# Optimization experiments

Hardware: AMD Instinct MI355X
Metric: run time of the kernel (lower is better)

## Reference

```python
import jax, jax.numpy as jnp
import numpy as np
from jax import lax

_DN = ('NCHW', 'OIHW', 'NCHW')


def _box1(s, k):
    # Separable box sum (all-ones kxk kernel) on a single-channel map (B,1,H,W).
    pad = (k - 1) // 2
    kh = jnp.ones((1, 1, k, 1), s.dtype)
    kw = jnp.ones((1, 1, 1, k), s.dtype)
    y = lax.conv_general_dilated(s, kh, (1, 1), [(pad, pad), (0, 0)], dimension_numbers=_DN)
    return lax.conv_general_dilated(y, kw, (1, 1), [(0, 0), (pad, pad)], dimension_numbers=_DN)


def _cgf(x, y, k, eps):
    # ConvGuidedFilterDlicate with weight-1 Conv2d(C,C,k): every output channel of
    # box_filter(t) equals box_sum(t.sum(channels)), so we keep channel dim = 1 and broadcast.
    B, C, H, W = x.shape
    Nc = C * _box1(jnp.ones((1, 1, H, W), x.dtype), k)           # box_filter(ones(1,C,H,W))
    mean_x = _box1(x.sum(1, keepdims=True), k) / Nc              # (B,1,H,W)
    mean_y = _box1(y.sum(1, keepdims=True), k) / Nc
    cov_xy = _box1((x * y).sum(1, keepdims=True), k) / Nc - mean_x * mean_y
    var_x = _box1((x * x).sum(1, keepdims=True), k) / Nc - mean_x * mean_x
    A = cov_xy / (var_x + eps)
    b = mean_y - A * mean_x
    # torch's A/b have C identical channels; box_filter then sums them -> factor C.
    mean_A = C * _box1(A, k)
    mean_b = C * _box1(b, k)
    return mean_A * y + mean_b                                   # broadcasts to (B,C,H,W)


def setup_inputs() -> dict:
    key = jax.random.key(0)
    k1, k2 = jax.random.split(key)
    x_hr = jax.random.normal(k1, (16, 3, 512, 512), jnp.float32)
    w1 = jax.random.normal(k2, (3, 9), jnp.float32) * 0.1        # conv1 weight (O, 3*nin1)
    return {"x_hr": x_hr, "w1": w1}


def reference(x_hr, w1):
    F1 = _cgf(x_hr, x_hr, 3, 0.16)
    F2 = _cgf(F1, F1, 7, 0.04)
    F3 = _cgf(F2, F2, 15, 0.01)
    D = jnp.concatenate([x_hr - F1, F1 - F2, F2 - F3], axis=1)   # (B,9,H,W)
    return jnp.einsum('oi,bihw->bohw', w1, D)                    # 1x1 conv, no bias
```

## Files before the change

### kernel.cpp

```cpp
#include <hip/hip_runtime.h>

#define BB 16
#define CC 3
#define HH 512
#define WW 512
#define HWP (HH*WW)
#define NMAP ((size_t)BB*HWP)

template <int P, int CH, int MODE>
__global__ __launch_bounds__(512, (MODE == 3 ? 2 : 4))
void stage(const float* __restrict__ xin, const float2* __restrict__ sqin,
           float2* __restrict__ abo, float2* __restrict__ sqo,
           const float2* __restrict__ ab1, const float2* __restrict__ ab2,
           const float* __restrict__ w1, float* __restrict__ outp, float eps)
{
    constexpr int RD  = 2*P + 1;
    constexpr int LW  = 512 + 2*P;
    constexpr int NCH = HH / CH;
    __shared__ float2 eA[LW];
    __shared__ float2 eB[LW];

    const int t  = threadIdx.x;
    const int bx = blockIdx.x;
    const int b  = bx / NCH;
    const int h0 = (bx % NCH) * CH;
    const size_t mapbase = (size_t)b * HWP;
    const float*  xb  = (MODE != 2) ? (xin + (size_t)b * CC * HWP) : nullptr;
    const float2* sqb = (MODE != 1) ? (sqin + mapbase) : nullptr;

    if (t < 2*P) {
        int sl = (t < P) ? t : (512 + t);
        eA[sl] = make_float2(0.f, 0.f);
        eB[sl] = make_float2(0.f, 0.f);
    }

    const int w   = t;
    const int wlo = (w - P < 0) ? 0 : w - P;
    const int whi = (w + P > WW-1) ? WW-1 : w + P;
    const float rcw = 1.0f / (float)(whi - wlo + 1);

    float cs0 = 0.f, cs1 = 0.f;
    float ca  = 0.f, cb  = 0.f;
    float rA[RD], rB[RD];

    auto loadSQ = [&](int rr, float& sv, float& qv) {
        size_t o = (size_t)rr * WW + w;
        if constexpr (MODE == 1) {
            float x0 = xb[o], x1 = xb[o + HWP], x2 = xb[o + 2*HWP];
            sv = x0 + x1 + x2;
            qv = x0*x0 + x1*x1 + x2*x2;
        } else {
            float2 v = sqb[o];
            sv = v.x; qv = v.y;
        }
    };

    auto advance = [&](int r) {
        int rin = r + P, rout = r - P - 1;
        if (rin < HH)  { float sv, qv; loadSQ(rin,  sv, qv); cs0 += sv; cs1 += qv; }
        if (rout >= 0) { float sv, qv; loadSQ(rout, sv, qv); cs0 -= sv; cs1 -= qv; }
    };

    auto phase1 = [&](int r, float& Aout, float& Bout) {
        eA[t + P] = make_float2(cs0, cs1);
        __syncthreads();
        float hs0 = 0.f, hs1 = 0.f;
#pragma unroll
        for (int d = 0; d <= 2*P; ++d) { float2 v = eA[t + d]; hs0 += v.x; hs1 += v.y; }
        __syncthreads();
        int rlo = (r - P < 0) ? 0 : r - P;
        int rhi = (r + P > HH-1) ? HH-1 : r + P;
        float rNc  = (1.f/3.f) * rcw / (float)(rhi - rlo + 1);
        float mean = hs0 * rNc;
        float var  = hs1 * rNc - mean * mean;
        float A    = var / (var + eps);
        Aout = A;
        Bout = mean * (1.f - A);
    };

    float w1r[27];
    if constexpr (MODE == 3) {
#pragma unroll
        for (int k = 0; k < 27; ++k) w1r[k] = w1[k];
    }

#pragma unroll
    for (int d = 0; d <= 2*P; ++d) {
        int rr = h0 - 2*P + d;
        if (rr >= 0) { float sv, qv; loadSQ(rr, sv, qv); cs0 += sv; cs1 += qv; }
    }

#pragma unroll
    for (int j = 0; j < 2*P; ++j) {
        int r = h0 - P + j;
        if (j > 0) advance(r);
        float A = 0.f, Bv = 0.f;
        if (r >= 0) { phase1(r, A, Bv); ca += A; cb += Bv; }
        rA[j % RD] = A; rB[j % RD] = Bv;
    }

#pragma unroll
    for (int i = 0; i < CH; ++i) {
        int r = h0 + P + i;
        int h = h0 + i;
        advance(r);
        float A = 0.f, Bv = 0.f;
        if (r < HH) { phase1(r, A, Bv); ca += A; cb += Bv; }
        rA[(2*P + i) % RD] = A; rB[(2*P + i) % RD] = Bv;

        eB[t + P] = make_float2(ca, cb);
        __syncthreads();
        float sA = 0.f, sB = 0.f;
#pragma unroll
        for (int d = 0; d <= 2*P; ++d) { float2 v = eB[t + d]; sA += v.x; sB += v.y; }
        __syncthreads();

        size_t oi = mapbase + (size_t)h * WW + w;
        if constexpr (MODE != 3) {
            abo[oi] = make_float2(sA, sB);
            float sv, qv; loadSQ(h, sv, qv);
            float mA = 3.f * sA, mb = 3.f * sB;
            sqo[oi] = make_float2(mA*sv + 3.f*mb,
                                  mA*mA*qv + 2.f*mA*mb*sv + 3.f*mb*mb);
        } else {
            float a3 = 3.f*sA, b3 = 3.f*sB;
            float2 v1 = ab1[oi], v2 = ab2[oi];
            float a1 = 3.f*v1.x, b1 = 3.f*v1.y;
            float a2 = 3.f*v2.x, b2 = 3.f*v2.y;
            float P1 = a1,      Q1 = b1;
            float P2 = a2 * P1, Q2 = a2 * Q1 + b2;
            float P3 = a3 * P2, Q3 = a3 * Q2 + b3;
            float alpha[3] = {1.f - P1, P1 - P2, P2 - P3};
            float beta[3]  = {-Q1,      Q1 - Q2, Q2 - Q3};
            size_t xo = (size_t)h * WW + w;
            float xv0 = xb[xo], xv1 = xb[xo + HWP], xv2 = xb[xo + 2*HWP];
#pragma unroll
            for (int o = 0; o < 3; ++o) {
                float acc = 0.f;
#pragma unroll
                for (int g = 0; g < 3; ++g) {
                    float w0v = w1r[o*9 + g*3 + 0];
                    float wv1 = w1r[o*9 + g*3 + 1];
                    float w2v = w1r[o*9 + g*3 + 2];
                    acc += alpha[g] * (w0v*xv0 + wv1*xv1 + w2v*xv2)
                         + beta[g]  * (w0v + wv1 + w2v);
                }
                outp[(size_t)b * CC * HWP + (size_t)o * HWP + xo] = acc;
            }
        }
        ca -= rA[i % RD]; cb -= rB[i % RD];
    }
}

extern "C" void kernel_launch(void* const* d_in, const int* in_sizes, int n_in,
                              void* d_out, int out_size, void* d_ws, size_t ws_size,
                              hipStream_t stream) {
    (void)in_sizes; (void)n_in; (void)out_size; (void)ws_size;
    const float* x  = (const float*)d_in[0];
    const float* w1 = (const float*)d_in[1];
    float* out = (float*)d_out;

    float2* sq1 = (float2*)d_ws;
    float2* sq2 = sq1 + NMAP;
    float2* ab1 = sq2 + NMAP;
    float2* ab2 = ab1 + NMAP;

    dim3 bl(512);
    dim3 g(BB * (HH / 16));

    stage<1,16,1><<<g, bl, 0, stream>>>(x, nullptr, ab1, sq1,
                                        nullptr, nullptr, nullptr, nullptr, 0.16f);
    stage<3,16,2><<<g, bl, 0, stream>>>(nullptr, sq1, ab2, sq2,
                                        nullptr, nullptr, nullptr, nullptr, 0.04f);
    stage<7,16,3><<<g, bl, 0, stream>>>(x, sq2, nullptr, nullptr,
                                        ab1, ab2, w1, out, 0.01f);
}
```

Baseline: 220.7 us.

## Process two columns per thread and merge both box-filter passes into one sync round

Each thread now handles two adjacent columns with 256-thread blocks, using vectorised float2/float4 loads and stores. The horizontal box sums for the (sum, sq) statistics and for the (A, b) coefficients are computed from shared memory in a single sync pair per row instead of two. The loop is software-pipelined so the next row's global loads are issued before the shared-memory exchange. Stages 1 and 2 also move to 8-row chunks, which adds halo recomputation in exchange for more blocks.

```diff
diff --git a/kernel.cpp b/kernel.cpp
--- a/kernel.cpp
+++ b/kernel.cpp
@@ -8,17 +8,21 @@
 #define NMAP ((size_t)BB*HWP)
 
 template <int P, int CH, int MODE>
-__global__ __launch_bounds__(512, (MODE == 3 ? 2 : 4))
+__global__ __launch_bounds__(256, MODE == 3 ? 2 : 4)
 void stage(const float* __restrict__ xin, const float2* __restrict__ sqin,
            float2* __restrict__ abo, float2* __restrict__ sqo,
-           const float2* __restrict__ ab1, const float2* __restrict__ ab2,
-           const float* __restrict__ w1, float* __restrict__ outp, float eps)
+           const float2* __restrict__ abp1, const float2* __restrict__ abp2,
+           const float* __restrict__ wt, float* __restrict__ outp, float eps)
 {
     constexpr int RD  = 2*P + 1;
-    constexpr int LW  = 512 + 2*P;
+    constexpr int HE  = (P+1)/2;
+    constexpr int NIT = CH + 2*P + 1;
     constexpr int NCH = HH / CH;
-    __shared__ float2 eA[LW];
-    __shared__ float2 eB[LW];
+    constexpr int mm  = (P-1)/2;
+    constexpr int MM  = (P+1)/2;
+
+    __shared__ float4 ev[256 + 2*HE];
+    __shared__ float4 od[256 + 2*HE];
 
     const int t  = threadIdx.x;
     const int bx = blockIdx.x;
@@ -28,127 +32,163 @@
     const float*  xb  = (MODE != 2) ? (xin + (size_t)b * CC * HWP) : nullptr;
     const float2* sqb = (MODE != 1) ? (sqin + mapbase) : nullptr;
 
-    if (t < 2*P) {
-        int sl = (t < P) ? t : (512 + t);
-        eA[sl] = make_float2(0.f, 0.f);
-        eB[sl] = make_float2(0.f, 0.f);
-    }
-
-    const int w   = t;
-    const int wlo = (w - P < 0) ? 0 : w - P;
-    const int whi = (w + P > WW-1) ? WW-1 : w + P;
-    const float rcw = 1.0f / (float)(whi - wlo + 1);
-
-    float cs0 = 0.f, cs1 = 0.f;
-    float ca  = 0.f, cb  = 0.f;
-    float rA[RD], rB[RD];
-
-    auto loadSQ = [&](int rr, float& sv, float& qv) {
-        size_t o = (size_t)rr * WW + w;
+    if (t < 2*HE) {
+        int sl = (t < HE) ? t : 256 + t;
+        ev[sl] = make_float4(0.f, 0.f, 0.f, 0.f);
+        od[sl] = make_float4(0.f, 0.f, 0.f, 0.f);
+    }
+
+    const int wc0 = 2*t;
+    const int wc1 = wc0 + 1;
+    const int wlo0 = (wc0-P < 0) ? 0 : wc0-P, whi0 = (wc0+P > WW-1) ? WW-1 : wc0+P;
+    const int wlo1 = (wc1-P < 0) ? 0 : wc1-P, whi1 = (wc1+P > WW-1) ? WW-1 : wc1+P;
+    const float rcw0 = 1.0f / (float)(whi0 - wlo0 + 1);
+    const float rcw1 = 1.0f / (float)(whi1 - wlo1 + 1);
+
+    float2 cs0 = make_float2(0.f,0.f), cs1 = make_float2(0.f,0.f);
+    float2 ca0 = make_float2(0.f,0.f), ca1 = make_float2(0.f,0.f);
+    float2 rg0[RD], rg1[RD];
+#pragma unroll
+    for (int k = 0; k < RD; ++k) { rg0[k] = make_float2(0.f,0.f); rg1[k] = make_float2(0.f,0.f); }
+
+    auto loadrow = [&](int rr, float2& d0, float2& d1) {
         if constexpr (MODE == 1) {
-            float x0 = xb[o], x1 = xb[o + HWP], x2 = xb[o + 2*HWP];
-            sv = x0 + x1 + x2;
-            qv = x0*x0 + x1*x1 + x2*x2;
+            size_t o = (size_t)rr * WW + wc0;
+            float2 x0 = *(const float2*)(xb + o);
+            float2 x1 = *(const float2*)(xb + o + HWP);
+            float2 x2 = *(const float2*)(xb + o + 2*HWP);
+            d0 = make_float2(x0.x+x1.x+x2.x, x0.x*x0.x + x1.x*x1.x + x2.x*x2.x);
+            d1 = make_float2(x0.y+x1.y+x2.y, x0.y*x0.y + x1.y*x1.y + x2.y*x2.y);
         } else {
-            float2 v = sqb[o];
-            sv = v.x; qv = v.y;
+            float4 v = ((const float4*)(sqb + (size_t)rr * WW))[t];
+            d0 = make_float2(v.x, v.y);
+            d1 = make_float2(v.z, v.w);
         }
     };
 
-    auto advance = [&](int r) {
-        int rin = r + P, rout = r - P - 1;
-        if (rin < HH)  { float sv, qv; loadSQ(rin,  sv, qv); cs0 += sv; cs1 += qv; }
-        if (rout >= 0) { float sv, qv; loadSQ(rout, sv, qv); cs0 -= sv; cs1 -= qv; }
-    };
-
-    auto phase1 = [&](int r, float& Aout, float& Bout) {
-        eA[t + P] = make_float2(cs0, cs1);
-        __syncthreads();
-        float hs0 = 0.f, hs1 = 0.f;
-#pragma unroll
-        for (int d = 0; d <= 2*P; ++d) { float2 v = eA[t + d]; hs0 += v.x; hs1 += v.y; }
-        __syncthreads();
-        int rlo = (r - P < 0) ? 0 : r - P;
-        int rhi = (r + P > HH-1) ? HH-1 : r + P;
-        float rNc  = (1.f/3.f) * rcw / (float)(rhi - rlo + 1);
-        float mean = hs0 * rNc;
-        float var  = hs1 * rNc - mean * mean;
-        float A    = var / (var + eps);
-        Aout = A;
-        Bout = mean * (1.f - A);
-    };
+#pragma unroll
+    for (int d = 0; d <= 2*P; ++d) {
+        int rr = h0 - 2*P + d;
+        if (rr >= 0) {
+            float2 d0, d1; loadrow(rr, d0, d1);
+            cs0.x += d0.x; cs0.y += d0.y; cs1.x += d1.x; cs1.y += d1.y;
+        }
+    }
 
     float w1r[27];
     if constexpr (MODE == 3) {
 #pragma unroll
-        for (int k = 0; k < 27; ++k) w1r[k] = w1[k];
-    }
-
-#pragma unroll
-    for (int d = 0; d <= 2*P; ++d) {
-        int rr = h0 - 2*P + d;
-        if (rr >= 0) { float sv, qv; loadSQ(rr, sv, qv); cs0 += sv; cs1 += qv; }
-    }
-
-#pragma unroll
-    for (int j = 0; j < 2*P; ++j) {
-        int r = h0 - P + j;
-        if (j > 0) advance(r);
-        float A = 0.f, Bv = 0.f;
-        if (r >= 0) { phase1(r, A, Bv); ca += A; cb += Bv; }
-        rA[j % RD] = A; rB[j % RD] = Bv;
-    }
-
-#pragma unroll
-    for (int i = 0; i < CH; ++i) {
-        int r = h0 + P + i;
-        int h = h0 + i;
-        advance(r);
-        float A = 0.f, Bv = 0.f;
-        if (r < HH) { phase1(r, A, Bv); ca += A; cb += Bv; }
-        rA[(2*P + i) % RD] = A; rB[(2*P + i) % RD] = Bv;
-
-        eB[t + P] = make_float2(ca, cb);
+        for (int k = 0; k < 27; ++k) w1r[k] = wt[k];
+    }
+
+#pragma unroll
+    for (int j = 0; j < NIT; ++j) {
+        const int r = h0 - P + j;
+
+        float2 gi0 = make_float2(0.f,0.f), gi1 = make_float2(0.f,0.f);
+        float2 go0 = make_float2(0.f,0.f), go1 = make_float2(0.f,0.f);
+        if (j < NIT-1) {
+            int rin = r + 1 + P, rout = r - P;
+            if (rin < HH)  loadrow(rin, gi0, gi1);
+            if (rout >= 0) loadrow(rout, go0, go1);
+        }
+
+        ev[HE+t] = make_float4(cs0.x, cs0.y, ca0.x, ca0.y);
+        od[HE+t] = make_float4(cs1.x, cs1.y, ca1.x, ca1.y);
         __syncthreads();
-        float sA = 0.f, sB = 0.f;
-#pragma unroll
-        for (int d = 0; d <= 2*P; ++d) { float2 v = eB[t + d]; sA += v.x; sB += v.y; }
+
+        float4 CE = make_float4(0.f,0.f,0.f,0.f), CO = make_float4(0.f,0.f,0.f,0.f);
+#pragma unroll
+        for (int i = -mm; i <= mm; ++i) {
+            float4 e = ev[HE+t+i], o = od[HE+t+i];
+            CE.x += e.x; CE.y += e.y; CE.z += e.z; CE.w += e.w;
+            CO.x += o.x; CO.y += o.y; CO.z += o.z; CO.w += o.w;
+        }
+        float4 eM = ev[HE+t+MM], oM = od[HE+t-MM];
         __syncthreads();
 
-        size_t oi = mapbase + (size_t)h * WW + w;
-        if constexpr (MODE != 3) {
-            abo[oi] = make_float2(sA, sB);
-            float sv, qv; loadSQ(h, sv, qv);
-            float mA = 3.f * sA, mb = 3.f * sB;
-            sqo[oi] = make_float2(mA*sv + 3.f*mb,
-                                  mA*mA*qv + 2.f*mA*mb*sv + 3.f*mb*mb);
-        } else {
-            float a3 = 3.f*sA, b3 = 3.f*sB;
-            float2 v1 = ab1[oi], v2 = ab2[oi];
-            float a1 = 3.f*v1.x, b1 = 3.f*v1.y;
-            float a2 = 3.f*v2.x, b2 = 3.f*v2.y;
-            float P1 = a1,      Q1 = b1;
-            float P2 = a2 * P1, Q2 = a2 * Q1 + b2;
-            float P3 = a3 * P2, Q3 = a3 * Q2 + b3;
-            float alpha[3] = {1.f - P1, P1 - P2, P2 - P3};
-            float beta[3]  = {-Q1,      Q1 - Q2, Q2 - Q3};
-            size_t xo = (size_t)h * WW + w;
-            float xv0 = xb[xo], xv1 = xb[xo + HWP], xv2 = xb[xo + 2*HWP];
-#pragma unroll
-            for (int o = 0; o < 3; ++o) {
-                float acc = 0.f;
-#pragma unroll
-                for (int g = 0; g < 3; ++g) {
-                    float w0v = w1r[o*9 + g*3 + 0];
-                    float wv1 = w1r[o*9 + g*3 + 1];
-                    float w2v = w1r[o*9 + g*3 + 2];
-                    acc += alpha[g] * (w0v*xv0 + wv1*xv1 + w2v*xv2)
-                         + beta[g]  * (w0v + wv1 + w2v);
+        float4 S0 = make_float4(CE.x+CO.x+oM.x, CE.y+CO.y+oM.y, CE.z+CO.z+oM.z, CE.w+CO.w+oM.w);
+        float4 S1 = make_float4(CE.x+CO.x+eM.x, CE.y+CO.y+eM.y, CE.z+CO.z+eM.z, CE.w+CO.w+eM.w);
+
+        if (j >= 2*P+1) {
+            const int h = r - P - 1;
+            const size_t oi = (size_t)h * WW + wc0;
+            if constexpr (MODE != 3) {
+                *((float4*)(abo + mapbase + oi)) = make_float4(S0.z, S0.w, S1.z, S1.w);
+                float2 d0, d1; loadrow(h, d0, d1);
+                float mA0 = 3.f*S0.z, mb0 = 3.f*S0.w;
+                float mA1 = 3.f*S1.z, mb1 = 3.f*S1.w;
+                *((float4*)(sqo + mapbase + oi)) = make_float4(
+                    mA0*d0.x + 3.f*mb0,
+                    mA0*mA0*d0.y + 2.f*mA0*mb0*d0.x + 3.f*mb0*mb0,
+                    mA1*d1.x + 3.f*mb1,
+                    mA1*mA1*d1.y + 2.f*mA1*mb1*d1.x + 3.f*mb1*mb1);
+            } else {
+                float4 v1 = *((const float4*)(abp1 + mapbase + oi));
+                float4 v2 = *((const float4*)(abp2 + mapbase + oi));
+                float2 xc0 = *(const float2*)(xb + oi);
+                float2 xc1 = *(const float2*)(xb + oi + HWP);
+                float2 xc2 = *(const float2*)(xb + oi + 2*HWP);
+                float res0[3], res1[3];
+#pragma unroll
+                for (int c = 0; c < 2; ++c) {
+                    float a1 = 3.f * (c ? v1.z : v1.x), b1 = 3.f * (c ? v1.w : v1.y);
+                    float a2 = 3.f * (c ? v2.z : v2.x), b2 = 3.f * (c ? v2.w : v2.y);
+                    float a3 = 3.f * (c ? S1.z : S0.z), b3 = 3.f * (c ? S1.w : S0.w);
+                    float x0 = c ? xc0.y : xc0.x;
+                    float x1 = c ? xc1.y : xc1.x;
+                    float x2 = c ? xc2.y : xc2.x;
+                    float Pp1 = a1,       Q1 = b1;
+                    float Pp2 = a2 * Pp1, Q2 = a2 * Q1 + b2;
+                    float Pp3 = a3 * Pp2, Q3 = a3 * Q2 + b3;
+                    float al[3] = {1.f - Pp1, Pp1 - Pp2, Pp2 - Pp3};
+                    float be[3] = {-Q1,       Q1 - Q2,   Q2 - Q3};
+                    float* rr_ = c ? res1 : res0;
+#pragma unroll
+                    for (int o = 0; o < 3; ++o) {
+                        float acc = 0.f;
+#pragma unroll
+                        for (int g = 0; g < 3; ++g) {
+                            float wa = w1r[o*9 + g*3 + 0];
+                            float wb = w1r[o*9 + g*3 + 1];
+                            float wc = w1r[o*9 + g*3 + 2];
+                            acc += al[g] * (wa*x0 + wb*x1 + wc*x2)
+                                 + be[g] * (wa + wb + wc);
+                        }
+                        rr_[o] = acc;
+                    }
                 }
-                outp[(size_t)b * CC * HWP + (size_t)o * HWP + xo] = acc;
+                float* ob = outp + (size_t)b * CC * HWP + oi;
+#pragma unroll
+                for (int o = 0; o < 3; ++o)
+                    *((float2*)(ob + (size_t)o * HWP)) = make_float2(res0[o], res1[o]);
             }
         }
-        ca -= rA[i % RD]; cb -= rB[i % RD];
+
+        if (j < NIT-1) {
+            float2 A0 = make_float2(0.f,0.f), A1 = make_float2(0.f,0.f);
+            if ((unsigned)r < (unsigned)HH) {
+                const int rlo = (r-P < 0) ? 0 : r-P;
+                const int rhi = (r+P > HH-1) ? HH-1 : r+P;
+                const float rch = 1.0f / (float)(rhi - rlo + 1);
+                const float rN0 = (1.f/3.f) * rcw0 * rch;
+                const float rN1 = (1.f/3.f) * rcw1 * rch;
+                float mean0 = S0.x * rN0;
+                float var0  = S0.y * rN0 - mean0*mean0;
+                float a0    = var0 / (var0 + eps);
+                A0 = make_float2(a0, mean0 * (1.f - a0));
+                float mean1 = S1.x * rN1;
+                float var1  = S1.y * rN1 - mean1*mean1;
+                float a1v   = var1 / (var1 + eps);
+                A1 = make_float2(a1v, mean1 * (1.f - a1v));
+            }
+            const int ri = j % RD;
+            ca0.x += A0.x - rg0[ri].x; ca0.y += A0.y - rg0[ri].y;
+            ca1.x += A1.x - rg1[ri].x; ca1.y += A1.y - rg1[ri].y;
+            rg0[ri] = A0; rg1[ri] = A1;
+            cs0.x += gi0.x - go0.x; cs0.y += gi0.y - go0.y;
+            cs1.x += gi1.x - go1.x; cs1.y += gi1.y - go1.y;
+        }
     }
 }
 
@@ -165,13 +205,12 @@
     float2* ab1 = sq2 + NMAP;
     float2* ab2 = ab1 + NMAP;
 
-    dim3 bl(512);
-    dim3 g(BB * (HH / 16));
-
-    stage<1,16,1><<<g, bl, 0, stream>>>(x, nullptr, ab1, sq1,
+    dim3 bl(256);
+
+    stage<1,8,1><<<dim3(BB*(HH/8)), bl, 0, stream>>>(x, nullptr, ab1, sq1,
                                         nullptr, nullptr, nullptr, nullptr, 0.16f);
-    stage<3,16,2><<<g, bl, 0, stream>>>(nullptr, sq1, ab2, sq2,
+    stage<3,8,2><<<dim3(BB*(HH/8)), bl, 0, stream>>>(nullptr, sq1, ab2, sq2,
                                         nullptr, nullptr, nullptr, nullptr, 0.04f);
-    stage<7,16,3><<<g, bl, 0, stream>>>(x, sq2, nullptr, nullptr,
+    stage<7,16,3><<<dim3(BB*(HH/16)), bl, 0, stream>>>(x, sq2, nullptr, nullptr,
                                         ab1, ab2, w1, out, 0.01f);
 }
```

Measured after the change: 199.6 us. 9.6% less time.

## Fuse first two guided-filter stages into one pipelined kernel with 2 columns per thread

Applied to the files above, without the earlier changes.

Merges stages 1 and 2 into a single kernel that streams rows, computing stage-1 A/b and then feeding the stage-2 box sums in a row pipeline. This removes the intermediate sq1 map's global round trip and one launch. Each thread now handles two columns with vectorized float4 loads and stores, horizontal sums use double-buffered shared memory with one barrier per row, and block IDs are swizzled. The cost is higher register pressure, more halo recomputation across row chunks, and a more complex pipeline with more room for indexing errors.

```diff
diff --git a/kernel.cpp b/kernel.cpp
--- a/kernel.cpp
+++ b/kernel.cpp
@@ -1,154 +1,300 @@
 #include <hip/hip_runtime.h>
 
 #define BB 16
-#define CC 3
 #define HH 512
 #define WW 512
 #define HWP (HH*WW)
 #define NMAP ((size_t)BB*HWP)
 
-template <int P, int CH, int MODE>
-__global__ __launch_bounds__(512, (MODE == 3 ? 2 : 4))
-void stage(const float* __restrict__ xin, const float2* __restrict__ sqin,
-           float2* __restrict__ abo, float2* __restrict__ sqo,
-           const float2* __restrict__ ab1, const float2* __restrict__ ab2,
-           const float* __restrict__ w1, float* __restrict__ outp, float eps)
+struct __align__(16) V4 { float x, y, z, w; };
+__device__ __forceinline__ V4 v4(float a, float b, float c, float d) { V4 r; r.x=a; r.y=b; r.z=c; r.w=d; return r; }
+__device__ __forceinline__ V4 v4z() { return v4(0.f,0.f,0.f,0.f); }
+__device__ __forceinline__ V4 vadd(V4 a, V4 b) { return v4(a.x+b.x, a.y+b.y, a.z+b.z, a.w+b.w); }
+__device__ __forceinline__ V4 vsub(V4 a, V4 b) { return v4(a.x-b.x, a.y-b.y, a.z-b.z, a.w-b.w); }
+
+template <int CH>
+__global__ __launch_bounds__(256, 2)
+void k1(const float* __restrict__ x, float2* __restrict__ sq2o,
+        float2* __restrict__ pq1o, float2* __restrict__ pq2o)
 {
-    constexpr int RD  = 2*P + 1;
-    constexpr int LW  = 512 + 2*P;
+    constexpr int NIT = CH + 17;
     constexpr int NCH = HH / CH;
-    __shared__ float2 eA[LW];
-    __shared__ float2 eB[LW];
+    __shared__ V4 G1[2][514];
+    __shared__ V4 G2[2][518];
 
     const int t  = threadIdx.x;
-    const int bx = blockIdx.x;
-    const int b  = bx / NCH;
-    const int h0 = (bx % NCH) * CH;
-    const size_t mapbase = (size_t)b * HWP;
-    const float*  xb  = (MODE != 2) ? (xin + (size_t)b * CC * HWP) : nullptr;
-    const float2* sqb = (MODE != 1) ? (sqin + mapbase) : nullptr;
-
-    if (t < 2*P) {
-        int sl = (t < P) ? t : (512 + t);
-        eA[sl] = make_float2(0.f, 0.f);
-        eB[sl] = make_float2(0.f, 0.f);
-    }
-
-    const int w   = t;
-    const int wlo = (w - P < 0) ? 0 : w - P;
-    const int whi = (w + P > WW-1) ? WW-1 : w + P;
-    const float rcw = 1.0f / (float)(whi - wlo + 1);
-
-    float cs0 = 0.f, cs1 = 0.f;
-    float ca  = 0.f, cb  = 0.f;
-    float rA[RD], rB[RD];
-
-    auto loadSQ = [&](int rr, float& sv, float& qv) {
-        size_t o = (size_t)rr * WW + w;
-        if constexpr (MODE == 1) {
-            float x0 = xb[o], x1 = xb[o + HWP], x2 = xb[o + 2*HWP];
-            sv = x0 + x1 + x2;
-            qv = x0*x0 + x1*x1 + x2*x2;
-        } else {
-            float2 v = sqb[o];
-            sv = v.x; qv = v.y;
-        }
+    const int c0 = 2 * t, c1 = c0 + 1;
+    int bid = blockIdx.x;
+    bid = (bid & 7) * ((BB * NCH) / 8) + (bid >> 3);
+    const int b  = bid / NCH;
+    const int h0 = (bid % NCH) * CH;
+    const size_t mb_ = (size_t)b * HWP;
+    const float* xb = x + (size_t)b * 3 * HWP;
+
+    if (t < 16) {
+        int bf = t & 1, s = t >> 1;
+        if (s < 2) G1[bf][s ? 513 : 0] = v4z();
+        else { int p = s - 2; G2[bf][p < 3 ? p : (515 + p - 3)] = v4z(); }
+    }
+
+    auto cwf = [&](int c, int P) -> float {
+        int lo = c - P < 0 ? 0 : c - P, hi = c + P > WW-1 ? WW-1 : c + P;
+        return (float)(hi - lo + 1);
     };
-
-    auto advance = [&](int r) {
-        int rin = r + P, rout = r - P - 1;
-        if (rin < HH)  { float sv, qv; loadSQ(rin,  sv, qv); cs0 += sv; cs1 += qv; }
-        if (rout >= 0) { float sv, qv; loadSQ(rout, sv, qv); cs0 -= sv; cs1 -= qv; }
+    const float cw10 = cwf(c0,1), cw11 = cwf(c1,1);
+    const float cw20 = cwf(c0,3), cw21 = cwf(c1,3);
+
+    V4 xr[5], h1r[3], s1r[9], h2r[7];
+#pragma unroll
+    for (int i = 0; i < 5; ++i) xr[i] = v4z();
+#pragma unroll
+    for (int i = 0; i < 3; ++i) h1r[i] = v4z();
+#pragma unroll
+    for (int i = 0; i < 9; ++i) s1r[i] = v4z();
+#pragma unroll
+    for (int i = 0; i < 7; ++i) h2r[i] = v4z();
+    V4 cs1 = v4z(), cs2 = v4z(), ca1 = v4z(), ca2 = v4z(), pv1 = v4z(), pv2 = v4z();
+
+    auto ldx = [&](int r) -> V4 {
+        if ((unsigned)r >= (unsigned)HH) return v4z();
+        size_t o = (size_t)r * WW + c0;
+        float2 a0 = *(const float2*)(xb + o);
+        float2 a1 = *(const float2*)(xb + o + HWP);
+        float2 a2 = *(const float2*)(xb + o + 2*HWP);
+        return v4(a0.x+a1.x+a2.x, a0.x*a0.x + a1.x*a1.x + a2.x*a2.x,
+                  a0.y+a1.y+a2.y, a0.y*a0.y + a1.y*a1.y + a2.y*a2.y);
     };
 
-    auto phase1 = [&](int r, float& Aout, float& Bout) {
-        eA[t + P] = make_float2(cs0, cs1);
+#pragma unroll
+    for (int j = 0; j < 3; ++j) {
+        int r = h0 - 8 + j;
+        if (r >= 0) xr[1 + j] = ldx(r);
+    }
+    cs1 = vadd(vadd(xr[1], xr[2]), xr[3]);
+    __syncthreads();
+
+#pragma unroll
+    for (int kk = 0; kk < NIT; ++kk) {
+        const int k  = h0 - 7 + kk;
+        const int bf = kk & 1;
+        G1[bf][c0+1] = v4(cs1.x, cs1.y, pv1.x, pv1.y);
+        G1[bf][c0+2] = v4(cs1.z, cs1.w, pv1.z, pv1.w);
+        G2[bf][c0+3] = v4(cs2.x, cs2.y, pv2.x, pv2.y);
+        G2[bf][c0+4] = v4(cs2.z, cs2.w, pv2.z, pv2.w);
+        V4 nx = v4z();
+        if (kk < NIT - 1) nx = ldx(k + 2);
         __syncthreads();
-        float hs0 = 0.f, hs1 = 0.f;
-#pragma unroll
-        for (int d = 0; d <= 2*P; ++d) { float2 v = eA[t + d]; hs0 += v.x; hs1 += v.y; }
+
+        V4 ga = G1[bf][c0], gb = G1[bf][c0+1], gc = G1[bf][c0+2], gd = G1[bf][c0+3];
+        V4 W10 = vadd(vadd(ga, gb), gc);
+        V4 W11 = vadd(vadd(gb, gc), gd);
+        V4 g0 = G2[bf][c0],   g1 = G2[bf][c0+1], g2 = G2[bf][c0+2], g3 = G2[bf][c0+3];
+        V4 g4 = G2[bf][c0+4], g5 = G2[bf][c0+5], g6 = G2[bf][c0+6], g7 = G2[bf][c0+7];
+        V4 W20 = vadd(vadd(vadd(g0, g1), vadd(g2, g3)), vadd(vadd(g4, g5), g6));
+        V4 W21 = vadd(vsub(W20, g0), g7);
+
+        V4 A1n = v4z();
+        if ((unsigned)k < (unsigned)HH) {
+            int lo = k-1 < 0 ? 0 : k-1, hi = k+1 > HH-1 ? HH-1 : k+1;
+            float chh = (float)(hi - lo + 1);
+            float rn0 = 1.f/(3.f*chh*cw10), rn1 = 1.f/(3.f*chh*cw11);
+            float m0 = W10.x*rn0, m1 = W11.x*rn1;
+            float v0 = W10.y*rn0 - m0*m0, v1 = W11.y*rn1 - m1*m1;
+            float a0 = v0/(v0 + 0.16f), a1 = v1/(v1 + 0.16f);
+            A1n = v4(a0, m0*(1.f-a0), a1, m1*(1.f-a1));
+        }
+        V4 HA1 = v4(W10.z, W10.w, W11.z, W11.w);
+        ca1 = vadd(ca1, vsub(HA1, h1r[kk % 3])); h1r[kk % 3] = HA1;
+
+        V4 xv = xr[kk % 5];
+        float mA0 = 3.f*ca1.x, mb0 = 3.f*ca1.y, mA1c = 3.f*ca1.z, mb1c = 3.f*ca1.w;
+        V4 s1n = v4z();
+        if ((unsigned)(k-2) < (unsigned)HH) {
+            s1n = v4(mA0*xv.x + 3.f*mb0,
+                     mA0*mA0*xv.y + 2.f*mA0*mb0*xv.x + 3.f*mb0*mb0,
+                     mA1c*xv.z + 3.f*mb1c,
+                     mA1c*mA1c*xv.w + 2.f*mA1c*mb1c*xv.z + 3.f*mb1c*mb1c);
+        }
+        if (kk >= 9 && kk <= CH + 8) {
+            size_t o = mb_ + (size_t)(k-2) * WW + c0;
+            *((float4*)&pq1o[o]) = make_float4(mA0, mb0, mA1c, mb1c);
+        }
+
+        V4 A2n = v4z();
+        {
+            int r2 = k - 6;
+            if ((unsigned)r2 < (unsigned)HH) {
+                int lo = r2-3 < 0 ? 0 : r2-3, hi = r2+3 > HH-1 ? HH-1 : r2+3;
+                float chh = (float)(hi - lo + 1);
+                float rn0 = 1.f/(3.f*chh*cw20), rn1 = 1.f/(3.f*chh*cw21);
+                float m0 = W20.x*rn0, m1 = W21.x*rn1;
+                float v0 = W20.y*rn0 - m0*m0, v1 = W21.y*rn1 - m1*m1;
+                float a0 = v0/(v0 + 0.04f), a1 = v1/(v1 + 0.04f);
+                A2n = v4(a0, m0*(1.f-a0), a1, m1*(1.f-a1));
+            }
+        }
+        V4 HA2 = v4(W20.z, W20.w, W21.z, W21.w);
+        ca2 = vadd(ca2, vsub(HA2, h2r[kk % 7])); h2r[kk % 7] = HA2;
+
+        if (kk >= 17 && kk <= CH + 16) {
+            V4 s1v = s1r[(kk + 1) % 9];
+            float a2  = 3.f*ca2.x, b2  = 3.f*ca2.y;
+            float a2c = 3.f*ca2.z, b2c = 3.f*ca2.w;
+            size_t o = mb_ + (size_t)(k-10) * WW + c0;
+            *((float4*)&sq2o[o]) = make_float4(
+                a2*s1v.x + 3.f*b2,
+                a2*a2*s1v.y + 2.f*a2*b2*s1v.x + 3.f*b2*b2,
+                a2c*s1v.z + 3.f*b2c,
+                a2c*a2c*s1v.w + 2.f*a2c*b2c*s1v.z + 3.f*b2c*b2c);
+            *((float4*)&pq2o[o]) = make_float4(a2, b2, a2c, b2c);
+        }
+
+        if (kk < NIT - 1) {
+            cs2 = vadd(cs2, vsub(s1n, s1r[(kk + 2) % 9]));
+            s1r[kk % 9] = s1n;
+            cs1 = vadd(cs1, vsub(nx, xr[(kk + 1) % 5]));
+            xr[(kk + 4) % 5] = nx;
+            pv1 = A1n; pv2 = A2n;
+        }
+    }
+}
+
+template <int CH>
+__global__ __launch_bounds__(256, 2)
+void k2(const float2* __restrict__ sq2, const float2* __restrict__ pq1,
+        const float2* __restrict__ pq2, const float* __restrict__ x,
+        const float* __restrict__ wt, float* __restrict__ outp)
+{
+    constexpr int NIT = CH + 15;
+    constexpr int NCH = HH / CH;
+    __shared__ V4 G3[2][526];
+
+    const int t  = threadIdx.x;
+    const int c0 = 2 * t, c1 = c0 + 1;
+    int bid = blockIdx.x;
+    bid = (bid & 7) * ((BB * NCH) / 8) + (bid >> 3);
+    const int b  = bid / NCH;
+    const int h0 = (bid % NCH) * CH;
+    const size_t mb_ = (size_t)b * HWP;
+    const float2* sb = sq2 + mb_;
+    const float*  xb = x + (size_t)b * 3 * HWP;
+    float* ob = outp + (size_t)b * 3 * HWP;
+
+    if (t < 28) {
+        int bf = t & 1, s = t >> 1;
+        G3[bf][s < 7 ? s : (519 + s - 7)] = v4z();
+    }
+    auto cwf = [&](int c) -> float {
+        int lo = c - 7 < 0 ? 0 : c - 7, hi = c + 7 > WW-1 ? WW-1 : c + 7;
+        return (float)(hi - lo + 1);
+    };
+    const float cw30 = cwf(c0), cw31 = cwf(c1);
+
+    float wr[27];
+#pragma unroll
+    for (int i = 0; i < 27; ++i) wr[i] = wt[i];
+
+    V4 h3r[15];
+#pragma unroll
+    for (int i = 0; i < 15; ++i) h3r[i] = v4z();
+    V4 cs3 = v4z(), ca3 = v4z(), pv3 = v4z();
+
+    auto lds2 = [&](int r) -> V4 {
+        if ((unsigned)r >= (unsigned)HH) return v4z();
+        float4 v = *((const float4*)&sb[(size_t)r * WW + c0]);
+        return v4(v.x, v.y, v.z, v.w);
+    };
+
+#pragma unroll
+    for (int j = 0; j < 15; ++j) cs3 = vadd(cs3, lds2(h0 - 14 + j));
+    __syncthreads();
+
+#pragma unroll
+    for (int kk = 0; kk < NIT; ++kk) {
+        const int k  = h0 - 7 + kk;
+        const int bf = kk & 1;
+        G3[bf][c0+7] = v4(cs3.x, cs3.y, pv3.x, pv3.y);
+        G3[bf][c0+8] = v4(cs3.z, cs3.w, pv3.z, pv3.w);
+        V4 nin = v4z(), nout = v4z();
+        if (kk < NIT - 1) { nin = lds2(k + 8); nout = lds2(k - 7); }
+        float4 q1v = make_float4(0,0,0,0), q2v = make_float4(0,0,0,0);
+        float2 xe0 = make_float2(0,0), xe1 = xe0, xe2 = xe0;
+        if (kk >= 15) {
+            size_t o = mb_ + (size_t)(k-8) * WW + c0;
+            q1v = *((const float4*)&pq1[o]);
+            q2v = *((const float4*)&pq2[o]);
+            size_t xo = (size_t)(k-8) * WW + c0;
+            xe0 = *(const float2*)(xb + xo);
+            xe1 = *(const float2*)(xb + xo + HWP);
+            xe2 = *(const float2*)(xb + xo + 2*HWP);
+        }
         __syncthreads();
-        int rlo = (r - P < 0) ? 0 : r - P;
-        int rhi = (r + P > HH-1) ? HH-1 : r + P;
-        float rNc  = (1.f/3.f) * rcw / (float)(rhi - rlo + 1);
-        float mean = hs0 * rNc;
-        float var  = hs1 * rNc - mean * mean;
-        float A    = var / (var + eps);
-        Aout = A;
-        Bout = mean * (1.f - A);
-    };
-
-    float w1r[27];
-    if constexpr (MODE == 3) {
-#pragma unroll
-        for (int k = 0; k < 27; ++k) w1r[k] = w1[k];
-    }
-
-#pragma unroll
-    for (int d = 0; d <= 2*P; ++d) {
-        int rr = h0 - 2*P + d;
-        if (rr >= 0) { float sv, qv; loadSQ(rr, sv, qv); cs0 += sv; cs1 += qv; }
-    }
-
-#pragma unroll
-    for (int j = 0; j < 2*P; ++j) {
-        int r = h0 - P + j;
-        if (j > 0) advance(r);
-        float A = 0.f, Bv = 0.f;
-        if (r >= 0) { phase1(r, A, Bv); ca += A; cb += Bv; }
-        rA[j % RD] = A; rB[j % RD] = Bv;
-    }
-
-#pragma unroll
-    for (int i = 0; i < CH; ++i) {
-        int r = h0 + P + i;
-        int h = h0 + i;
-        advance(r);
-        float A = 0.f, Bv = 0.f;
-        if (r < HH) { phase1(r, A, Bv); ca += A; cb += Bv; }
-        rA[(2*P + i) % RD] = A; rB[(2*P + i) % RD] = Bv;
-
-        eB[t + P] = make_float2(ca, cb);
-        __syncthreads();
-        float sA = 0.f, sB = 0.f;
-#pragma unroll
-        for (int d = 0; d <= 2*P; ++d) { float2 v = eB[t + d]; sA += v.x; sB += v.y; }
-        __syncthreads();
-
-        size_t oi = mapbase + (size_t)h * WW + w;
-        if constexpr (MODE != 3) {
-            abo[oi] = make_float2(sA, sB);
-            float sv, qv; loadSQ(h, sv, qv);
-            float mA = 3.f * sA, mb = 3.f * sB;
-            sqo[oi] = make_float2(mA*sv + 3.f*mb,
-                                  mA*mA*qv + 2.f*mA*mb*sv + 3.f*mb*mb);
-        } else {
-            float a3 = 3.f*sA, b3 = 3.f*sB;
-            float2 v1 = ab1[oi], v2 = ab2[oi];
-            float a1 = 3.f*v1.x, b1 = 3.f*v1.y;
-            float a2 = 3.f*v2.x, b2 = 3.f*v2.y;
-            float P1 = a1,      Q1 = b1;
-            float P2 = a2 * P1, Q2 = a2 * Q1 + b2;
-            float P3 = a3 * P2, Q3 = a3 * Q2 + b3;
-            float alpha[3] = {1.f - P1, P1 - P2, P2 - P3};
-            float beta[3]  = {-Q1,      Q1 - Q2, Q2 - Q3};
-            size_t xo = (size_t)h * WW + w;
-            float xv0 = xb[xo], xv1 = xb[xo + HWP], xv2 = xb[xo + 2*HWP];
-#pragma unroll
-            for (int o = 0; o < 3; ++o) {
-                float acc = 0.f;
-#pragma unroll
-                for (int g = 0; g < 3; ++g) {
-                    float w0v = w1r[o*9 + g*3 + 0];
-                    float wv1 = w1r[o*9 + g*3 + 1];
-                    float w2v = w1r[o*9 + g*3 + 2];
-                    acc += alpha[g] * (w0v*xv0 + wv1*xv1 + w2v*xv2)
-                         + beta[g]  * (w0v + wv1 + w2v);
+
+        V4 g[16];
+#pragma unroll
+        for (int j = 0; j < 16; ++j) g[j] = G3[bf][c0 + j];
+        V4 s01 = vadd(g[0], g[1]),   s23 = vadd(g[2], g[3]);
+        V4 s45 = vadd(g[4], g[5]),   s67 = vadd(g[6], g[7]);
+        V4 s89 = vadd(g[8], g[9]),   sab = vadd(g[10], g[11]);
+        V4 scd = vadd(g[12], g[13]);
+        V4 W0 = vadd(vadd(vadd(s01, s23), vadd(s45, s67)),
+                     vadd(vadd(s89, sab), vadd(scd, g[14])));
+        V4 W1 = vadd(vsub(W0, g[0]), g[15]);
+
+        V4 A3n = v4z();
+        if ((unsigned)k < (unsigned)HH) {
+            int lo = k-7 < 0 ? 0 : k-7, hi = k+7 > HH-1 ? HH-1 : k+7;
+            float chh = (float)(hi - lo + 1);
+            float rn0 = 1.f/(3.f*chh*cw30), rn1 = 1.f/(3.f*chh*cw31);
+            float m0 = W0.x*rn0, m1 = W1.x*rn1;
+            float v0 = W0.y*rn0 - m0*m0, v1 = W1.y*rn1 - m1*m1;
+            float a0 = v0/(v0 + 0.01f), a1 = v1/(v1 + 0.01f);
+            A3n = v4(a0, m0*(1.f-a0), a1, m1*(1.f-a1));
+        }
+        V4 HA3 = v4(W0.z, W0.w, W1.z, W1.w);
+        ca3 = vadd(ca3, vsub(HA3, h3r[kk % 15])); h3r[kk % 15] = HA3;
+
+        if (kk >= 15) {
+            float a3  = 3.f*ca3.x, b3  = 3.f*ca3.y;
+            float a3c = 3.f*ca3.z, b3c = 3.f*ca3.w;
+            float r0[3], r1[3];
+#pragma unroll
+            for (int c = 0; c < 2; ++c) {
+                float P1 = c ? q1v.z : q1v.x, Q1 = c ? q1v.w : q1v.y;
+                float a2 = c ? q2v.z : q2v.x, b2 = c ? q2v.w : q2v.y;
+                float a3v = c ? a3c : a3,     b3v = c ? b3c : b3;
+                float P2 = a2 * P1,  Q2 = a2 * Q1 + b2;
+                float P3 = a3v * P2, Q3 = a3v * Q2 + b3v;
+                float al[3] = {1.f - P1, P1 - P2, P2 - P3};
+                float be[3] = {-Q1,      Q1 - Q2, Q2 - Q3};
+                float x0 = c ? xe0.y : xe0.x;
+                float x1 = c ? xe1.y : xe1.x;
+                float x2 = c ? xe2.y : xe2.x;
+                float* rr = c ? r1 : r0;
+#pragma unroll
+                for (int oc = 0; oc < 3; ++oc) {
+                    float acc = 0.f;
+#pragma unroll
+                    for (int gg = 0; gg < 3; ++gg) {
+                        float wa = wr[oc*9 + gg*3 + 0];
+                        float wb = wr[oc*9 + gg*3 + 1];
+                        float wc = wr[oc*9 + gg*3 + 2];
+                        acc += al[gg] * (wa*x0 + wb*x1 + wc*x2)
+                             + be[gg] * (wa + wb + wc);
+                    }
+                    rr[oc] = acc;
                 }
-                outp[(size_t)b * CC * HWP + (size_t)o * HWP + xo] = acc;
             }
-        }
-        ca -= rA[i % RD]; cb -= rB[i % RD];
+            size_t xo = (size_t)(k-8) * WW + c0;
+#pragma unroll
+            for (int oc = 0; oc < 3; ++oc)
+                *((float2*)(ob + (size_t)oc * HWP + xo)) = make_float2(r0[oc], r1[oc]);
+        }
+
+        if (kk < NIT - 1) {
+            cs3 = vadd(cs3, vsub(nin, nout));
+            pv3 = A3n;
+        }
     }
 }
 
@@ -160,18 +306,13 @@
     const float* w1 = (const float*)d_in[1];
     float* out = (float*)d_out;
 
-    float2* sq1 = (float2*)d_ws;
-    float2* sq2 = sq1 + NMAP;
-    float2* ab1 = sq2 + NMAP;
-    float2* ab2 = ab1 + NMAP;
-
-    dim3 bl(512);
-    dim3 g(BB * (HH / 16));
-
-    stage<1,16,1><<<g, bl, 0, stream>>>(x, nullptr, ab1, sq1,
-                                        nullptr, nullptr, nullptr, nullptr, 0.16f);
-    stage<3,16,2><<<g, bl, 0, stream>>>(nullptr, sq1, ab2, sq2,
-                                        nullptr, nullptr, nullptr, nullptr, 0.04f);
-    stage<7,16,3><<<g, bl, 0, stream>>>(x, sq2, nullptr, nullptr,
-                                        ab1, ab2, w1, out, 0.01f);
+    float2* sq2 = (float2*)d_ws;
+    float2* pq1 = sq2 + NMAP;
+    float2* pq2 = pq1 + NMAP;
+
+    constexpr int CH = 16;
+    dim3 bl(256), g(BB * (HH / CH));
+
+    k1<CH><<<g, bl, 0, stream>>>(x, sq2, pq1, pq2);
+    k2<CH><<<g, bl, 0, stream>>>(sq2, pq1, pq2, x, w1, out);
 }
```

Result: slower. 372.4 us (+68.7%).
